# Optimization experiments

Measured on AMD Instinct MI355X. Metric: run time of the kernel, lower is better.

The kernel has to match this reference:

```python
import jax, jax.numpy as jnp
import numpy as np

B, S, H, NH = 2, 2048, 1024, 16
HD = H // NH  # 64


def setup_inputs() -> dict:
    key = jax.random.key(0)
    ks = jax.random.split(key, 11)
    sc = 1.0 / np.sqrt(H)
    inp = {
        "q": jax.random.normal(ks[0], (B, S, H), dtype=jnp.float32),
        "k": jax.random.normal(ks[1], (B, S, H), dtype=jnp.float32),
        "v": jax.random.normal(ks[2], (B, S, H), dtype=jnp.float32),
        # nn.Linear params: weight [out,in], bias [out]
        "wq_w": jax.random.normal(ks[3], (H, H), dtype=jnp.float32) * sc,
        "wq_b": jnp.zeros((H,), dtype=jnp.float32),
        "wk_w": jax.random.normal(ks[4], (H, H), dtype=jnp.float32) * sc,
        "wk_b": jnp.zeros((H,), dtype=jnp.float32),
        "wv_w": jax.random.normal(ks[5], (H, H), dtype=jnp.float32) * sc,
        "wv_b": jnp.zeros((H,), dtype=jnp.float32),
        "wo_w": jax.random.normal(ks[6], (H, H), dtype=jnp.float32) * sc,
        "wo_b": jnp.zeros((H,), dtype=jnp.float32),
    }
    return inp


def _split_heads(x):
    # [B,S,H] -> [B,NH,S,HD]
    b, s, _ = x.shape
    return x.reshape(b, s, NH, HD).transpose(0, 2, 1, 3)


def reference(q, k, v, wq_w, wq_b, wk_w, wk_b, wv_w, wv_b, wo_w, wo_b):
    qw = q @ wq_w.T + wq_b
    kw = k @ wk_w.T + wk_b
    vw = v @ wv_w.T + wv_b
    hq = _split_heads(qw)  # [B,NH,S,HD]
    hk = _split_heads(kw)
    hv = _split_heads(vw)
    scale = 1.0 / jnp.sqrt(jnp.float32(HD))
    scores = jnp.einsum("bhqd,bhkd->bhqk", hq, hk) * scale  # [B,NH,S,S]
    attn = jax.nn.softmax(scores, axis=-1)
    out = jnp.einsum("bhqk,bhkd->bhqd", attn, hv)  # [B,NH,S,HD]
    out = out.transpose(0, 2, 1, 3).reshape(q.shape[0], -1, H)  # [B,S,H]
    final = out @ wo_w.T + wo_b
    return final, attn
```

## Files before the change

kernel.cpp:

```cpp
#include <hip/hip_runtime.h>

typedef short bf16x8 __attribute__((ext_vector_type(8)));
typedef float f32x4 __attribute__((ext_vector_type(4)));
typedef unsigned short ushort4v __attribute__((ext_vector_type(4)));
typedef unsigned short ushort8 __attribute__((ext_vector_type(8)));

#define DEVI static __device__ __forceinline__

DEVI unsigned short f2bf(float f) {
    unsigned u = __float_as_uint(f);
    u += 0x7FFFu + ((u >> 16) & 1u);
    return (unsigned short)(u >> 16);
}

typedef __attribute__((address_space(3))) unsigned int* lds_ptr_t;
typedef const __attribute__((address_space(1))) unsigned int* gbl_ptr_t;
#define GLDS(gp, lp) __builtin_amdgcn_global_load_lds((gbl_ptr_t)(gp), (lds_ptr_t)(lp), 16, 0, 0)

__global__ void cvt_kernel(const float* __restrict__ src, unsigned short* __restrict__ dst, int n) {
    int i = (blockIdx.x * 256 + threadIdx.x) * 4;
    if (i >= n) return;
    float4 v = *(const float4*)(src + i);
    ushort4v o;
    o.x = f2bf(v.x); o.y = f2bf(v.y); o.z = f2bf(v.z); o.w = f2bf(v.w);
    *(ushort4v*)(dst + i) = o;
}

__global__ void cvt2_kernel(const float* __restrict__ s0, unsigned short* __restrict__ d0, int n0,
                            const float* __restrict__ s1, unsigned short* __restrict__ d1, int n1) {
    int idx = blockIdx.x * 256 + threadIdx.x;
    const int c0 = n0 >> 2;
    const float* src; unsigned short* dst; int i;
    if (idx < c0) { src = s0; dst = d0; i = idx * 4; }
    else {
        i = (idx - c0) * 4;
        if (i >= n1) return;
        src = s1; dst = d1;
    }
    float4 v = *(const float4*)(src + i);
    ushort4v o;
    o.x = f2bf(v.x); o.y = f2bf(v.y); o.z = f2bf(v.z); o.w = f2bf(v.w);
    *(ushort4v*)(dst + i) = o;
}

template <int MODE>
__global__ __launch_bounds__(256) void gemm_bt(const unsigned short* __restrict__ A,
                                               const unsigned short* __restrict__ W,
                                               const float* __restrict__ bias,
                                               void* __restrict__ Cout) {
    constexpr int K = 1024;
    __shared__ unsigned short Asb[2][64 * 32];
    __shared__ unsigned short Bsb[2][128 * 32];
    const int t = threadIdx.x;
    const int w = t >> 6, l = t & 63;
    const int wr = w >> 1, wc = w & 1;
    const int fr = l & 15, fg = l >> 4;
    const int m0 = blockIdx.y * 64, n0 = blockIdx.x * 128;

    const int ra = t >> 2, qa = (t & 3) * 8;
    const int c1 = 256 + t, rb1 = c1 >> 2, qb1 = (c1 & 3) * 8;

    f32x4 acc[2][4] = {};

#define STG(kb, pb)                                                        \
    {                                                                      \
        GLDS(A + (size_t)(m0 + ra) * K + (kb) + qa, &Asb[pb][t * 8]);      \
        GLDS(W + (size_t)(n0 + ra) * K + (kb) + qa, &Bsb[pb][t * 8]);      \
        GLDS(W + (size_t)(n0 + rb1) * K + (kb) + qb1, &Bsb[pb][c1 * 8]);   \
    }

    STG(0, 0);
    for (int t2 = 0; t2 < 32; ++t2) {
        const int cur = t2 & 1;
        if (t2 < 31) {
            STG((t2 + 1) * 32, cur ^ 1);
            asm volatile("s_waitcnt vmcnt(3)" ::: "memory");
        } else {
            asm volatile("s_waitcnt vmcnt(0)" ::: "memory");
        }
        __syncthreads();
        bf16x8 af[2], bfv[4];
#pragma unroll
        for (int mi = 0; mi < 2; mi++)
            af[mi] = *(const bf16x8*)(&Asb[cur][(wr * 32 + mi * 16 + fr) * 32 + fg * 8]);
#pragma unroll
        for (int ni = 0; ni < 4; ni++)
            bfv[ni] = *(const bf16x8*)(&Bsb[cur][(wc * 64 + ni * 16 + fr) * 32 + fg * 8]);
#pragma unroll
        for (int mi = 0; mi < 2; mi++)
#pragma unroll
            for (int ni = 0; ni < 4; ni++)
                acc[mi][ni] = __builtin_amdgcn_mfma_f32_16x16x32_bf16(af[mi], bfv[ni], acc[mi][ni], 0, 0, 0);
        __syncthreads();
    }
#undef STG

#pragma unroll
    for (int ni = 0; ni < 4; ni++) {
        const int n = n0 + wc * 64 + ni * 16 + fr;
        const float bv = bias[n];
#pragma unroll
        for (int mi = 0; mi < 2; mi++) {
            const int mb = m0 + wr * 32 + mi * 16 + fg * 4;
            if constexpr (MODE == 1) {
                float* C = (float*)Cout;
#pragma unroll
                for (int r = 0; r < 4; r++) C[(size_t)(mb + r) * 1024 + n] = acc[mi][ni][r] + bv;
            } else if constexpr (MODE == 0) {
                unsigned short* C = (unsigned short*)Cout;
                const int h = n >> 6, hd = n & 63;
#pragma unroll
                for (int r = 0; r < 4; r++) {
                    const int m = mb + r;
                    const int bb = m >> 11, s = m & 2047;
                    C[(size_t)((bb * 16 + h) * 2048 + s) * 64 + hd] = f2bf(acc[mi][ni][r] + bv);
                }
            } else {
                unsigned short* C = (unsigned short*)Cout;
                const int h = n >> 6, hd = n & 63;
                const int bb = mb >> 11, s = mb & 2047;
                ushort4v pk;
                pk.x = f2bf(acc[mi][ni][0] + bv);
                pk.y = f2bf(acc[mi][ni][1] + bv);
                pk.z = f2bf(acc[mi][ni][2] + bv);
                pk.w = f2bf(acc[mi][ni][3] + bv);
                *(ushort4v*)(C + (size_t)((bb * 16 + h) * 64 + hd) * 2048 + s) = pk;
            }
        }
    }
}

__global__ __launch_bounds__(256, 4) void attn_kernel(const unsigned short* __restrict__ Qh,
                                                      const unsigned short* __restrict__ Kh,
                                                      const unsigned short* __restrict__ Vt,
                                                      unsigned short* __restrict__ Obuf,
                                                      float* __restrict__ AttnOut) {
    __shared__ char Plds[32768];
    __shared__ float rpart[32][4];
    __shared__ float rinv_s[32];

    const int qt = blockIdx.x, h = blockIdx.y, b = blockIdx.z;
    const int bh = b * 16 + h;
    const int q0 = qt * 32;
    const int t = threadIdx.x, w = t >> 6, l = t & 63;
    const int fr = l & 15, fg = l >> 4;
    const unsigned swz = (unsigned)((fr & 7) << 4);

    const unsigned short* qb = Qh + (size_t)(bh * 2048 + q0) * 64;
    bf16x8 qf[2][2];
#pragma unroll
    for (int qs = 0; qs < 2; qs++)
#pragma unroll
        for (int kc = 0; kc < 2; kc++)
            qf[qs][kc] = *(const bf16x8*)(qb + (size_t)(qs * 16 + fr) * 64 + kc * 32 + fg * 8);

    const unsigned short* kbase = Kh + (size_t)bh * 2048 * 64;
    const unsigned short* vtb = Vt + (size_t)bh * 64 * 2048;

    float s0 = 0.f, s1 = 0.f;
    for (int kt = 0; kt < 8; ++kt) {
        const int kb = w * 512 + kt * 64;
#pragma unroll
        for (int mt = 0; mt < 4; ++mt) {
            const unsigned short* kr = kbase + (size_t)(kb + mt * 16 + fr) * 64 + fg * 8;
            bf16x8 kf0 = *(const bf16x8*)kr;
            bf16x8 kf1 = *(const bf16x8*)(kr + 32);
            f32x4 d0 = {}, d1 = {};
            d0 = __builtin_amdgcn_mfma_f32_16x16x32_bf16(kf0, qf[0][0], d0, 0, 0, 0);
            d0 = __builtin_amdgcn_mfma_f32_16x16x32_bf16(kf1, qf[0][1], d0, 0, 0, 0);
            d1 = __builtin_amdgcn_mfma_f32_16x16x32_bf16(kf0, qf[1][0], d1, 0, 0, 0);
            d1 = __builtin_amdgcn_mfma_f32_16x16x32_bf16(kf1, qf[1][1], d1, 0, 0, 0);
#pragma unroll
            for (int r = 0; r < 4; r++) {
                s0 += __expf(d0[r] * 0.125f);
                s1 += __expf(d1[r] * 0.125f);
            }
        }
    }
    s0 += __shfl_xor(s0, 16, 64); s0 += __shfl_xor(s0, 32, 64);
    s1 += __shfl_xor(s1, 16, 64); s1 += __shfl_xor(s1, 32, 64);
    if (l < 16) { rpart[l][w] = s0; rpart[l + 16][w] = s1; }
    __syncthreads();
    if (t < 32) rinv_s[t] = 1.0f / (rpart[t][0] + rpart[t][1] + rpart[t][2] + rpart[t][3]);
    __syncthreads();
    const float ri0 = rinv_s[fr], ri1 = rinv_s[16 + fr];

    f32x4 opv[2][4] = {};
    float* attnB = AttnOut + (size_t)bh * 2048 * 2048;

#define STAGE(KT)                                                                                   \
    {                                                                                               \
        const int kb = w * 512 + (KT) * 64;                                                         \
        const unsigned pbase = (unsigned)((w + ((KT) & 1) * 4) * 4096);                             \
        _Pragma("unroll") for (int mt = 0; mt < 4; ++mt) {                                          \
            const unsigned short* kr = kbase + (size_t)(kb + mt * 16 + fr) * 64 + fg * 8;           \
            bf16x8 kf0 = *(const bf16x8*)kr;                                                        \
            bf16x8 kf1 = *(const bf16x8*)(kr + 32);                                                 \
            f32x4 d0 = {}, d1 = {};                                                                 \
            d0 = __builtin_amdgcn_mfma_f32_16x16x32_bf16(kf0, qf[0][0], d0, 0, 0, 0);               \
            d0 = __builtin_amdgcn_mfma_f32_16x16x32_bf16(kf1, qf[0][1], d0, 0, 0, 0);               \
            d1 = __builtin_amdgcn_mfma_f32_16x16x32_bf16(kf0, qf[1][0], d1, 0, 0, 0);               \
            d1 = __builtin_amdgcn_mfma_f32_16x16x32_bf16(kf1, qf[1][1], d1, 0, 0, 0);               \
            f32x4 p0, p1;                                                                           \
            _Pragma("unroll") for (int r = 0; r < 4; r++) {                                         \
                p0[r] = __expf(d0[r] * 0.125f) * ri0;                                               \
                p1[r] = __expf(d1[r] * 0.125f) * ri1;                                               \
            }                                                                                       \
            const int kcol = kb + mt * 16 + fg * 4;                                                 \
            __builtin_nontemporal_store(p0, (f32x4*)(attnB + (size_t)(q0 + fr) * 2048 + kcol));     \
            __builtin_nontemporal_store(p1, (f32x4*)(attnB + (size_t)(q0 + 16 + fr) * 2048 + kcol));\
            ushort4v pk0, pk1;                                                                      \
            _Pragma("unroll") for (int r = 0; r < 4; r++) { pk0[r] = f2bf(p0[r]); pk1[r] = f2bf(p1[r]); } \
            const unsigned colb = (unsigned)(mt * 32 + fg * 8) ^ swz;                               \
            *(ushort4v*)(Plds + pbase + (unsigned)fr * 128 + colb) = pk0;                           \
            *(ushort4v*)(Plds + pbase + (unsigned)(16 + fr) * 128 + colb) = pk1;                    \
        }                                                                                           \
    }

#define PVSTEP(KT)                                                                                  \
    {                                                                                               \
        const int kb = w * 512 + (KT) * 64;                                                         \
        const unsigned pbase = (unsigned)((w + ((KT) & 1) * 4) * 4096);                             \
        _Pragma("unroll") for (int kc = 0; kc < 2; ++kc) {                                          \
            const unsigned ro = (unsigned)(kc * 64 + fg * 16) ^ swz;                                \
            bf16x8 pa0 = *(const bf16x8*)(Plds + pbase + (unsigned)fr * 128 + ro);                  \
            bf16x8 pa1 = *(const bf16x8*)(Plds + pbase + (unsigned)(16 + fr) * 128 + ro);           \
            _Pragma("unroll") for (int dt = 0; dt < 4; ++dt) {                                      \
                bf16x8 vf = *(const bf16x8*)(vtb + (size_t)(dt * 16 + fr) * 2048 + kb + kc * 32 + fg * 8); \
                opv[0][dt] = __builtin_amdgcn_mfma_f32_16x16x32_bf16(pa0, vf, opv[0][dt], 0, 0, 0); \
                opv[1][dt] = __builtin_amdgcn_mfma_f32_16x16x32_bf16(pa1, vf, opv[1][dt], 0, 0, 0); \
            }                                                                                       \
        }                                                                                           \
    }

    STAGE(0);
    for (int kt = 1; kt < 8; ++kt) {
        STAGE(kt);
        PVSTEP(kt - 1);
    }
    PVSTEP(7);
#undef STAGE
#undef PVSTEP

    __syncthreads();
    float* ored = (float*)Plds;
    for (int i = t; i < 32 * 68; i += 256) ored[i] = 0.f;
    __syncthreads();
    for (int ww = 0; ww < 4; ++ww) {
        if (w == ww) {
#pragma unroll
            for (int qs = 0; qs < 2; qs++)
#pragma unroll
                for (int dt = 0; dt < 4; dt++)
#pragma unroll
                    for (int r = 0; r < 4; r++)
                        ored[(qs * 16 + fg * 4 + r) * 68 + dt * 16 + fr] += opv[qs][dt][r];
        }
        __syncthreads();
    }
    {
        const int row = t >> 3, cb = (t & 7) * 8;
        ushort8 pk;
#pragma unroll
        for (int j = 0; j < 8; j++) pk[j] = f2bf(ored[row * 68 + cb + j]);
        *(ushort8*)(Obuf + (size_t)(b * 2048 + q0 + row) * 1024 + h * 64 + cb) = pk;
    }
}

extern "C" void kernel_launch(void* const* d_in, const int* in_sizes, int n_in,
                              void* d_out, int out_size, void* d_ws, size_t ws_size,
                              hipStream_t stream) {
    const float* q = (const float*)d_in[0];
    const float* k = (const float*)d_in[1];
    const float* v = (const float*)d_in[2];
    const float* wqw = (const float*)d_in[3];
    const float* wqb = (const float*)d_in[4];
    const float* wkw = (const float*)d_in[5];
    const float* wkb = (const float*)d_in[6];
    const float* wvw = (const float*)d_in[7];
    const float* wvb = (const float*)d_in[8];
    const float* wow = (const float*)d_in[9];
    const float* wob = (const float*)d_in[10];

    char* ws = (char*)d_ws;
    unsigned short* xbf  = (unsigned short*)(ws);
    unsigned short* wbf  = (unsigned short*)(ws + 8388608);
    unsigned short* qh   = (unsigned short*)(ws + 10485760);
    unsigned short* kh   = (unsigned short*)(ws + 18874368);
    unsigned short* vt   = (unsigned short*)(ws + 27262976);
    unsigned short* obuf = (unsigned short*)(ws + 35651584);

    float* finalOut = (float*)d_out;
    float* attnOut = finalOut + 4194304;

    const int NX = 4194304, NW = 1048576;
    const int c2grid = (NX + NW) / 1024;
    dim3 gGrid(8, 64), aGrid(64, 16, 2);

    cvt2_kernel<<<c2grid, 256, 0, stream>>>(q, xbf, NX, wqw, wbf, NW);
    gemm_bt<0><<<gGrid, 256, 0, stream>>>(xbf, wbf, wqb, qh);

    cvt2_kernel<<<c2grid, 256, 0, stream>>>(k, xbf, NX, wkw, wbf, NW);
    gemm_bt<0><<<gGrid, 256, 0, stream>>>(xbf, wbf, wkb, kh);

    cvt2_kernel<<<c2grid, 256, 0, stream>>>(v, xbf, NX, wvw, wbf, NW);
    gemm_bt<2><<<gGrid, 256, 0, stream>>>(xbf, wbf, wvb, vt);

    attn_kernel<<<aGrid, 256, 0, stream>>>(qh, kh, vt, obuf, attnOut);

    cvt_kernel<<<NW / 1024, 256, 0, stream>>>(wow, wbf, NW);
    gemm_bt<1><<<gGrid, 256, 0, stream>>>(obuf, wbf, wob, finalOut);
}
```

Measured before the change: 332.0 us.

## Keep unnormalized bf16 probabilities in registers, feed PV MFMA directly without LDS

Measured after the change: 368.1 us. +10.9%, slower.

```diff
diff --git a/kernel.cpp b/kernel.cpp
--- a/kernel.cpp
+++ b/kernel.cpp
@@ -11,6 +11,12 @@
     unsigned u = __float_as_uint(f);
     u += 0x7FFFu + ((u >> 16) & 1u);
     return (unsigned short)(u >> 16);
+}
+
+DEVI unsigned cvtpk(float lo, float hi) {
+    unsigned r;
+    asm("v_cvt_pk_bf16_f32 %0, %1, %2" : "=v"(r) : "v"(lo), "v"(hi));
+    return r;
 }
 
 typedef __attribute__((address_space(3))) unsigned int* lds_ptr_t;
@@ -119,151 +125,118 @@
                 unsigned short* C = (unsigned short*)Cout;
                 const int h = n >> 6, hd = n & 63;
                 const int bb = mb >> 11, s = mb & 2047;
+                const int blk = s >> 6, off = s & 63;
+                const int pos = blk * 64 + (off >> 5) * 32 + ((off & 15) >> 2) * 8 + ((off >> 4) & 1) * 4;
                 ushort4v pk;
                 pk.x = f2bf(acc[mi][ni][0] + bv);
                 pk.y = f2bf(acc[mi][ni][1] + bv);
                 pk.z = f2bf(acc[mi][ni][2] + bv);
                 pk.w = f2bf(acc[mi][ni][3] + bv);
-                *(ushort4v*)(C + (size_t)((bb * 16 + h) * 64 + hd) * 2048 + s) = pk;
+                *(ushort4v*)(C + (size_t)((bb * 16 + h) * 64 + hd) * 2048 + pos) = pk;
             }
         }
     }
 }
 
-__global__ __launch_bounds__(256, 4) void attn_kernel(const unsigned short* __restrict__ Qh,
+__global__ __launch_bounds__(256, 3) void attn_kernel(const unsigned short* __restrict__ Qh,
                                                       const unsigned short* __restrict__ Kh,
                                                       const unsigned short* __restrict__ Vt,
                                                       unsigned short* __restrict__ Obuf,
                                                       float* __restrict__ AttnOut) {
-    __shared__ char Plds[32768];
-    __shared__ float rpart[32][4];
-    __shared__ float rinv_s[32];
-
-    const int qt = blockIdx.x, h = blockIdx.y, b = blockIdx.z;
-    const int bh = b * 16 + h;
-    const int q0 = qt * 32;
+    __shared__ float rpart[16][4];
+    __shared__ float rinv_s[16];
+    __shared__ float ored[16][68];
+
+    const int i = blockIdx.x;
+    const int bh = (i & 7) * 4 + (i >> 10);
+    const int q0 = ((i >> 3) & 127) * 16;
+    const int b = bh >> 4, h = bh & 15;
     const int t = threadIdx.x, w = t >> 6, l = t & 63;
     const int fr = l & 15, fg = l >> 4;
-    const unsigned swz = (unsigned)((fr & 7) << 4);
+    const float SCL = 0.1803368801111f;
 
     const unsigned short* qb = Qh + (size_t)(bh * 2048 + q0) * 64;
-    bf16x8 qf[2][2];
-#pragma unroll
-    for (int qs = 0; qs < 2; qs++)
-#pragma unroll
-        for (int kc = 0; kc < 2; kc++)
-            qf[qs][kc] = *(const bf16x8*)(qb + (size_t)(qs * 16 + fr) * 64 + kc * 32 + fg * 8);
-
-    const unsigned short* kbase = Kh + (size_t)bh * 2048 * 64;
+    const bf16x8 qf0 = *(const bf16x8*)(qb + (size_t)fr * 64 + fg * 8);
+    const bf16x8 qf1 = *(const bf16x8*)(qb + (size_t)fr * 64 + 32 + fg * 8);
+
+    const unsigned short* kbase = Kh + ((size_t)bh * 2048 + w * 512) * 64;
     const unsigned short* vtb = Vt + (size_t)bh * 64 * 2048;
 
-    float s0 = 0.f, s1 = 0.f;
+    unsigned p[8][8];
+    float rs = 0.f;
+#pragma unroll
     for (int kt = 0; kt < 8; ++kt) {
-        const int kb = w * 512 + kt * 64;
 #pragma unroll
         for (int mt = 0; mt < 4; ++mt) {
-            const unsigned short* kr = kbase + (size_t)(kb + mt * 16 + fr) * 64 + fg * 8;
+            const unsigned short* kr = kbase + (size_t)(kt * 64 + mt * 16 + fr) * 64 + fg * 8;
             bf16x8 kf0 = *(const bf16x8*)kr;
             bf16x8 kf1 = *(const bf16x8*)(kr + 32);
-            f32x4 d0 = {}, d1 = {};
-            d0 = __builtin_amdgcn_mfma_f32_16x16x32_bf16(kf0, qf[0][0], d0, 0, 0, 0);
-            d0 = __builtin_amdgcn_mfma_f32_16x16x32_bf16(kf1, qf[0][1], d0, 0, 0, 0);
-            d1 = __builtin_amdgcn_mfma_f32_16x16x32_bf16(kf0, qf[1][0], d1, 0, 0, 0);
-            d1 = __builtin_amdgcn_mfma_f32_16x16x32_bf16(kf1, qf[1][1], d1, 0, 0, 0);
-#pragma unroll
-            for (int r = 0; r < 4; r++) {
-                s0 += __expf(d0[r] * 0.125f);
-                s1 += __expf(d1[r] * 0.125f);
+            f32x4 d = {};
+            d = __builtin_amdgcn_mfma_f32_16x16x32_bf16(kf0, qf0, d, 0, 0, 0);
+            d = __builtin_amdgcn_mfma_f32_16x16x32_bf16(kf1, qf1, d, 0, 0, 0);
+            const float e0 = exp2f(d[0] * SCL), e1 = exp2f(d[1] * SCL);
+            const float e2 = exp2f(d[2] * SCL), e3 = exp2f(d[3] * SCL);
+            rs += (e0 + e1) + (e2 + e3);
+            p[kt][mt * 2] = cvtpk(e0, e1);
+            p[kt][mt * 2 + 1] = cvtpk(e2, e3);
+        }
+    }
+    rs += __shfl_xor(rs, 16, 64);
+    rs += __shfl_xor(rs, 32, 64);
+    if (l < 16) rpart[l][w] = rs;
+    __syncthreads();
+    for (int j = t; j < 16 * 68; j += 256) (&ored[0][0])[j] = 0.f;
+    if (t < 16) rinv_s[t] = 1.0f / (rpart[t][0] + rpart[t][1] + rpart[t][2] + rpart[t][3]);
+    __syncthreads();
+    const float ri = rinv_s[fr];
+
+    float* attnB = AttnOut + (size_t)bh * 2048 * 2048 + (size_t)(q0 + fr) * 2048 + w * 512;
+    f32x4 opv[4] = {};
+#pragma unroll
+    for (int kt = 0; kt < 8; ++kt) {
+#pragma unroll
+        for (int mt = 0; mt < 4; ++mt) {
+            const unsigned a = p[kt][mt * 2], c = p[kt][mt * 2 + 1];
+            f32x4 o;
+            o[0] = __uint_as_float(a << 16) * ri;
+            o[1] = __uint_as_float(a & 0xffff0000u) * ri;
+            o[2] = __uint_as_float(c << 16) * ri;
+            o[3] = __uint_as_float(c & 0xffff0000u) * ri;
+            __builtin_nontemporal_store(o, (f32x4*)(attnB + kt * 64 + mt * 16 + fg * 4));
+        }
+#pragma unroll
+        for (int kc = 0; kc < 2; ++kc) {
+            union { unsigned u[4]; bf16x8 v; } pb;
+            pb.u[0] = p[kt][4 * kc + 0];
+            pb.u[1] = p[kt][4 * kc + 1];
+            pb.u[2] = p[kt][4 * kc + 2];
+            pb.u[3] = p[kt][4 * kc + 3];
+#pragma unroll
+            for (int dt = 0; dt < 4; ++dt) {
+                bf16x8 vf = *(const bf16x8*)(vtb + (size_t)(dt * 16 + fr) * 2048 + w * 512 + kt * 64 + kc * 32 + fg * 8);
+                opv[dt] = __builtin_amdgcn_mfma_f32_16x16x32_bf16(vf, pb.v, opv[dt], 0, 0, 0);
             }
         }
     }
-    s0 += __shfl_xor(s0, 16, 64); s0 += __shfl_xor(s0, 32, 64);
-    s1 += __shfl_xor(s1, 16, 64); s1 += __shfl_xor(s1, 32, 64);
-    if (l < 16) { rpart[l][w] = s0; rpart[l + 16][w] = s1; }
-    __syncthreads();
-    if (t < 32) rinv_s[t] = 1.0f / (rpart[t][0] + rpart[t][1] + rpart[t][2] + rpart[t][3]);
-    __syncthreads();
-    const float ri0 = rinv_s[fr], ri1 = rinv_s[16 + fr];
-
-    f32x4 opv[2][4] = {};
-    float* attnB = AttnOut + (size_t)bh * 2048 * 2048;
-
-#define STAGE(KT)                                                                                   \
-    {                                                                                               \
-        const int kb = w * 512 + (KT) * 64;                                                         \
-        const unsigned pbase = (unsigned)((w + ((KT) & 1) * 4) * 4096);                             \
-        _Pragma("unroll") for (int mt = 0; mt < 4; ++mt) {                                          \
-            const unsigned short* kr = kbase + (size_t)(kb + mt * 16 + fr) * 64 + fg * 8;           \
-            bf16x8 kf0 = *(const bf16x8*)kr;                                                        \
-            bf16x8 kf1 = *(const bf16x8*)(kr + 32);                                                 \
-            f32x4 d0 = {}, d1 = {};                                                                 \
-            d0 = __builtin_amdgcn_mfma_f32_16x16x32_bf16(kf0, qf[0][0], d0, 0, 0, 0);               \
-            d0 = __builtin_amdgcn_mfma_f32_16x16x32_bf16(kf1, qf[0][1], d0, 0, 0, 0);               \
-            d1 = __builtin_amdgcn_mfma_f32_16x16x32_bf16(kf0, qf[1][0], d1, 0, 0, 0);               \
-            d1 = __builtin_amdgcn_mfma_f32_16x16x32_bf16(kf1, qf[1][1], d1, 0, 0, 0);               \
-            f32x4 p0, p1;                                                                           \
-            _Pragma("unroll") for (int r = 0; r < 4; r++) {                                         \
-                p0[r] = __expf(d0[r] * 0.125f) * ri0;                                               \
-                p1[r] = __expf(d1[r] * 0.125f) * ri1;                                               \
-            }                                                                                       \
-            const int kcol = kb + mt * 16 + fg * 4;                                                 \
-            __builtin_nontemporal_store(p0, (f32x4*)(attnB + (size_t)(q0 + fr) * 2048 + kcol));     \
-            __builtin_nontemporal_store(p1, (f32x4*)(attnB + (size_t)(q0 + 16 + fr) * 2048 + kcol));\
-            ushort4v pk0, pk1;                                                                      \
-            _Pragma("unroll") for (int r = 0; r < 4; r++) { pk0[r] = f2bf(p0[r]); pk1[r] = f2bf(p1[r]); } \
-            const unsigned colb = (unsigned)(mt * 32 + fg * 8) ^ swz;                               \
-            *(ushort4v*)(Plds + pbase + (unsigned)fr * 128 + colb) = pk0;                           \
-            *(ushort4v*)(Plds + pbase + (unsigned)(16 + fr) * 128 + colb) = pk1;                    \
-        }                                                                                           \
-    }
-
-#define PVSTEP(KT)                                                                                  \
-    {                                                                                               \
-        const int kb = w * 512 + (KT) * 64;                                                         \
-        const unsigned pbase = (unsigned)((w + ((KT) & 1) * 4) * 4096);                             \
-        _Pragma("unroll") for (int kc = 0; kc < 2; ++kc) {                                          \
-            const unsigned ro = (unsigned)(kc * 64 + fg * 16) ^ swz;                                \
-            bf16x8 pa0 = *(const bf16x8*)(Plds + pbase + (unsigned)fr * 128 + ro);                  \
-            bf16x8 pa1 = *(const bf16x8*)(Plds + pbase + (unsigned)(16 + fr) * 128 + ro);           \
-            _Pragma("unroll") for (int dt = 0; dt < 4; ++dt) {                                      \
-                bf16x8 vf = *(const bf16x8*)(vtb + (size_t)(dt * 16 + fr) * 2048 + kb + kc * 32 + fg * 8); \
-                opv[0][dt] = __builtin_amdgcn_mfma_f32_16x16x32_bf16(pa0, vf, opv[0][dt], 0, 0, 0); \
-                opv[1][dt] = __builtin_amdgcn_mfma_f32_16x16x32_bf16(pa1, vf, opv[1][dt], 0, 0, 0); \
-            }                                                                                       \
-        }                                                                                           \
-    }
-
-    STAGE(0);
-    for (int kt = 1; kt < 8; ++kt) {
-        STAGE(kt);
-        PVSTEP(kt - 1);
-    }
-    PVSTEP(7);
-#undef STAGE
-#undef PVSTEP
-
-    __syncthreads();
-    float* ored = (float*)Plds;
-    for (int i = t; i < 32 * 68; i += 256) ored[i] = 0.f;
+
     __syncthreads();
     for (int ww = 0; ww < 4; ++ww) {
         if (w == ww) {
 #pragma unroll
-            for (int qs = 0; qs < 2; qs++)
-#pragma unroll
-                for (int dt = 0; dt < 4; dt++)
-#pragma unroll
-                    for (int r = 0; r < 4; r++)
-                        ored[(qs * 16 + fg * 4 + r) * 68 + dt * 16 + fr] += opv[qs][dt][r];
+            for (int dt = 0; dt < 4; dt++)
+#pragma unroll
+                for (int r = 0; r < 4; r++)
+                    ored[fr][dt * 16 + 4 * fg + r] += opv[dt][r];
         }
         __syncthreads();
     }
     {
-        const int row = t >> 3, cb = (t & 7) * 8;
-        ushort8 pk;
-#pragma unroll
-        for (int j = 0; j < 8; j++) pk[j] = f2bf(ored[row * 68 + cb + j]);
-        *(ushort8*)(Obuf + (size_t)(b * 2048 + q0 + row) * 1024 + h * 64 + cb) = pk;
+        const int row = t >> 4, cb = (t & 15) * 4;
+        const float rr = rinv_s[row];
+        ushort4v pk;
+#pragma unroll
+        for (int j = 0; j < 4; j++) pk[j] = f2bf(ored[row][cb + j] * rr);
+        *(ushort4v*)(Obuf + (size_t)(b * 2048 + q0 + row) * 1024 + h * 64 + cb) = pk;
     }
 }
 
@@ -295,7 +268,7 @@
 
     const int NX = 4194304, NW = 1048576;
     const int c2grid = (NX + NW) / 1024;
-    dim3 gGrid(8, 64), aGrid(64, 16, 2);
+    dim3 gGrid(8, 64);
 
     cvt2_kernel<<<c2grid, 256, 0, stream>>>(q, xbf, NX, wqw, wbf, NW);
     gemm_bt<0><<<gGrid, 256, 0, stream>>>(xbf, wbf, wqb, qh);
@@ -306,7 +279,7 @@
     cvt2_kernel<<<c2grid, 256, 0, stream>>>(v, xbf, NX, wvw, wbf, NW);
     gemm_bt<2><<<gGrid, 256, 0, stream>>>(xbf, wbf, wvb, vt);
 
-    attn_kernel<<<aGrid, 256, 0, stream>>>(qh, kh, vt, obuf, attnOut);
+    attn_kernel<<<4096, 256, 0, stream>>>(qh, kh, vt, obuf, attnOut);
 
     cvt_kernel<<<NW / 1024, 256, 0, stream>>>(wow, wbf, NW);
     gemm_bt<1><<<gGrid, 256, 0, stream>>>(obuf, wbf, wob, finalOut);
```
